# Performance work log

Hardware: AMD Instinct MI355X
Metric: run time of the kernel (lower is better)

The kernel has to match this reference:

```python
import jax, jax.numpy as jnp
import numpy as np

B, LQ, LK = 4, 2048, 2048
DQ, DK, DO = 1024, 1024, 1024


def setup_inputs() -> dict:
    key = jax.random.key(0)
    ks = jax.random.split(key, 9)
    s = 0.02
    return {
        "query_input": jax.random.normal(ks[0], (B, LQ, DQ), jnp.float32),
        "key_input": jax.random.normal(ks[1], (B, LK, DK), jnp.float32),
        "value_input": jax.random.normal(ks[2], (B, LK, DK), jnp.float32),
        "Wq": jax.random.normal(ks[3], (DQ, DO), jnp.float32) * s,
        "bq": jax.random.normal(ks[4], (DO,), jnp.float32) * s,
        "Wk": jax.random.normal(ks[5], (DK, DO), jnp.float32) * s,
        "bk": jax.random.normal(ks[6], (DO,), jnp.float32) * s,
        "Wv": jax.random.normal(ks[7], (DK, DO), jnp.float32) * s,
        "bv": jax.random.normal(ks[8], (DO,), jnp.float32) * s,
    }


def reference(query_input, key_input, value_input, Wq, bq, Wk, bk, Wv, bv):
    scale = jnp.asarray(DO, query_input.dtype) ** 0.5
    q = query_input @ Wq + bq              # [B, Lq, D]
    k = key_input @ Wk + bk                # [B, Lk, D]
    v = value_input @ Wv + bv              # [B, Lk, D]
    attn = jnp.einsum("bqd,bkd->bqk", q, k) / scale
    attn = jax.nn.softmax(attn, axis=-1)
    return jnp.einsum("bqk,bkd->bqd", attn, v)
```

## Files before the change

kernel.cpp:

```cpp
#include <hip/hip_runtime.h>

typedef _Float16 f16x8 __attribute__((ext_vector_type(8)));
typedef _Float16 f16x4 __attribute__((ext_vector_type(4)));
typedef float f32x4 __attribute__((ext_vector_type(4)));
typedef int   v4i   __attribute__((ext_vector_type(4)));

__device__ __forceinline__ void lds_load16(const _Float16* g, _Float16* l) {
    __builtin_amdgcn_global_load_lds(
        (const __attribute__((address_space(1))) void*)g,
        (__attribute__((address_space(3))) void*)l,
        16, 0, 0);
}

__device__ __forceinline__ f16x8 ldsr(unsigned a) {
    v4i r;
    asm volatile("ds_read_b128 %0, %1" : "=v"(r) : "v"(a));
    return __builtin_bit_cast(f16x8, r);
}

template <int MODE>
__global__ __launch_bounds__(512, 2)
void gemm_core(const _Float16* A0, const _Float16* B0, void* C0, const float* b0,
               const _Float16* A1, const _Float16* B1, void* C1, const float* b1,
               const _Float16* A2, const _Float16* B2, void* C2, const float* b2,
               float* rowsum)
{
    constexpr int BM  = (MODE == 5) ? 128 : 256;
    constexpr int K   = (MODE == 5) ? 2048 : 1024;
    constexpr int LDA = (MODE == 5) ? 2048 : 1024;
    constexpr int LDB = (MODE == 5) ? 8192 : 1024;
    constexpr int NT  = K / 64;
    constexpr int MI  = BM / 32;
    constexpr int MH  = MI / 2;
    constexpr int LA  = BM / 64;
    constexpr int LT  = LA + 4;

    __shared__ __align__(16) _Float16 As[2][BM * 64];
    __shared__ __align__(16) _Float16 Bs[2][256 * 64];

    const int z_ = blockIdx.z;
    const int bx = blockIdx.x, by = blockIdx.y;
    const int t    = threadIdx.x;
    const int w    = t >> 6;
    const int lane = t & 63;
    const int ln   = lane & 15;
    const int kq   = lane >> 4;
    const int wm   = (w >> 2) * (BM / 2);
    const int wn   = (w & 3) * 64;

    const _Float16* A;
    const _Float16* B;
    size_t cbase = 0;
    int m0, n0, z = z_;

    if (MODE == 0) {
        A = z == 0 ? A0 : z == 1 ? A1 : A2;
        B = z == 0 ? B0 : z == 1 ? B1 : B2;
        if (z == 2) { m0 = (by & 3) * 256;             n0 = (bx * 4 + (by >> 2)) * 256; }
        else        { m0 = (bx * 4 + (by >> 2)) * 256; n0 = (by & 3) * 256; }
    } else if (MODE == 3) {
        A = A0 + (size_t)z * 2048 * 1024;
        B = B0 + (size_t)z * 2048 * 1024;
        cbase = (size_t)z * 2048 * 2048;
        rowsum += z * 2048;
        m0 = ((bx & 3) * 2 + (by >> 2)) * 256;
        n0 = ((bx >> 2) * 4 + (by & 3)) * 256;
    } else {
        z = (blockIdx.z << 1) | (bx >> 2);
        A = A0 + (size_t)z * 2048 * 2048;
        B = B0 + (size_t)z * 2048;
        cbase = (size_t)z * 2048 * 1024;
        rowsum += z * 2048;
        m0 = by * 128;
        n0 = (bx & 3) * 256;
    }

    const int r6 = t >> 3;
    const int cw = ((t & 7) ^ (r6 & 7)) * 8;
    const _Float16* gA = A + (size_t)(m0 + r6) * LDA + cw;
    const _Float16* gB = B + (size_t)(n0 + r6) * LDB + cw;

    auto stA = [&](int b, int kt, int s) {
        lds_load16(gA + (size_t)(s * 64) * LDA + kt * 64, As[b] + s * 4096 + w * 512);
    };
    auto stB = [&](int b, int kt, int s) {
        lds_load16(gB + (size_t)(s * 64) * LDB + kt * 64, Bs[b] + s * 4096 + w * 512);
    };

    const int xr  = ln & 7;
    const int sk0 = ((0 + kq) ^ xr) * 8;
    const int sk1 = ((4 + kq) ^ xr) * 8;
    const int ra  = (wm + ln) * 64;
    const int rb  = (wn + ln) * 64;

    const unsigned uA0 = (unsigned)(uintptr_t)(__attribute__((address_space(3))) _Float16*)&As[0][0];
    const unsigned uA1 = (unsigned)(uintptr_t)(__attribute__((address_space(3))) _Float16*)&As[1][0];
    const unsigned uB0 = (unsigned)(uintptr_t)(__attribute__((address_space(3))) _Float16*)&Bs[0][0];
    const unsigned uB1 = (unsigned)(uintptr_t)(__attribute__((address_space(3))) _Float16*)&Bs[1][0];
    const unsigned aA[2][2] = { { uA0 + 2u * (ra + sk0), uA0 + 2u * (ra + sk1) },
                                { uA1 + 2u * (ra + sk0), uA1 + 2u * (ra + sk1) } };
    const unsigned aB[2][2] = { { uB0 + 2u * (rb + sk0), uB0 + 2u * (rb + sk1) },
                                { uB1 + 2u * (rb + sk0), uB1 + 2u * (rb + sk1) } };

    f16x8 af[MH][2], bf[4][2];
    f32x4 acc[MI][4] = {};

    {
#pragma unroll
        for (int s = 0; s < LA; ++s) stA(0, 0, s);
#pragma unroll
        for (int s = 0; s < 4; ++s)  stB(0, 0, s);
#pragma unroll
        for (int s = 0; s < LA; ++s) stA(1, 1, s);
#pragma unroll
        for (int s = 0; s < 4; ++s)  stB(1, 1, s);
    }
    if constexpr (MODE == 5) asm volatile("s_waitcnt vmcnt(6)" ::: "memory");
    else                     asm volatile("s_waitcnt vmcnt(8)" ::: "memory");
    __builtin_amdgcn_s_barrier();
    __builtin_amdgcn_sched_barrier(0);

#pragma unroll 2
    for (int kc = 0; kc < NT; ++kc) {
        const int  b  = kc & 1;
        const bool pf = (kc + 2 < NT);

#pragma unroll
        for (int i = 0; i < MH; ++i) {
            af[i][0] = ldsr(aA[b][0] + i * 2048);
            af[i][1] = ldsr(aA[b][1] + i * 2048);
        }
#pragma unroll
        for (int j = 0; j < 2; ++j) {
            bf[j][0] = ldsr(aB[b][0] + j * 2048);
            bf[j][1] = ldsr(aB[b][1] + j * 2048);
        }
        __builtin_amdgcn_s_barrier();
        asm volatile("s_waitcnt lgkmcnt(0)" ::: "memory");
        __builtin_amdgcn_sched_barrier(0);
        __builtin_amdgcn_s_setprio(1);
#pragma unroll
        for (int kh = 0; kh < 2; ++kh)
#pragma unroll
            for (int i = 0; i < MH; ++i)
#pragma unroll
                for (int j = 0; j < 2; ++j)
                    acc[i][j] = __builtin_amdgcn_mfma_f32_16x16x32_f16(af[i][kh], bf[j][kh], acc[i][j], 0, 0, 0);
        __builtin_amdgcn_s_setprio(0);
        __builtin_amdgcn_s_barrier();
        __builtin_amdgcn_sched_barrier(0);

#pragma unroll
        for (int j = 2; j < 4; ++j) {
            bf[j][0] = ldsr(aB[b][0] + j * 2048);
            bf[j][1] = ldsr(aB[b][1] + j * 2048);
        }
        if constexpr (LA == 4) {
            if (pf) { stA(b, kc + 2, 0); stA(b, kc + 2, 2); }
        }
        __builtin_amdgcn_s_barrier();
        asm volatile("s_waitcnt lgkmcnt(0)" ::: "memory");
        __builtin_amdgcn_sched_barrier(0);
        __builtin_amdgcn_s_setprio(1);
#pragma unroll
        for (int kh = 0; kh < 2; ++kh)
#pragma unroll
            for (int i = 0; i < MH; ++i)
#pragma unroll
                for (int j = 2; j < 4; ++j)
                    acc[i][j] = __builtin_amdgcn_mfma_f32_16x16x32_f16(af[i][kh], bf[j][kh], acc[i][j], 0, 0, 0);
        __builtin_amdgcn_s_setprio(0);
        __builtin_amdgcn_s_barrier();
        __builtin_amdgcn_sched_barrier(0);

#pragma unroll
        for (int i = 0; i < MH; ++i) {
            af[i][0] = ldsr(aA[b][0] + (i + MH) * 2048);
            af[i][1] = ldsr(aA[b][1] + (i + MH) * 2048);
        }
        if (pf) { stB(b, kc + 2, 0); stB(b, kc + 2, 1); stB(b, kc + 2, 2); }
        __builtin_amdgcn_s_barrier();
        asm volatile("s_waitcnt lgkmcnt(0)" ::: "memory");
        __builtin_amdgcn_sched_barrier(0);
        __builtin_amdgcn_s_setprio(1);
#pragma unroll
        for (int kh = 0; kh < 2; ++kh)
#pragma unroll
            for (int i = 0; i < MH; ++i)
#pragma unroll
                for (int j = 0; j < 2; ++j)
                    acc[i + MH][j] = __builtin_amdgcn_mfma_f32_16x16x32_f16(af[i][kh], bf[j][kh], acc[i + MH][j], 0, 0, 0);
        __builtin_amdgcn_s_setprio(0);
        __builtin_amdgcn_s_barrier();
        __builtin_amdgcn_sched_barrier(0);

        if (pf) {
            stB(b, kc + 2, 3);
            if constexpr (LA == 4) { stA(b, kc + 2, 1); stA(b, kc + 2, 3); }
            else                   { stA(b, kc + 2, 0); stA(b, kc + 2, 1); }
            if constexpr (MODE == 5) asm volatile("s_waitcnt vmcnt(6)" ::: "memory");
            else                     asm volatile("s_waitcnt vmcnt(8)" ::: "memory");
        } else if (kc + 1 < NT) {
            asm volatile("s_waitcnt vmcnt(0)" ::: "memory");
        }
        __builtin_amdgcn_s_barrier();
        __builtin_amdgcn_sched_barrier(0);
        __builtin_amdgcn_s_setprio(1);
#pragma unroll
        for (int kh = 0; kh < 2; ++kh)
#pragma unroll
            for (int i = 0; i < MH; ++i)
#pragma unroll
                for (int j = 2; j < 4; ++j)
                    acc[i + MH][j] = __builtin_amdgcn_mfma_f32_16x16x32_f16(af[i][kh], bf[j][kh], acc[i + MH][j], 0, 0, 0);
        __builtin_amdgcn_s_setprio(0);
        __builtin_amdgcn_s_barrier();
        __builtin_amdgcn_sched_barrier(0);
    }

    if (MODE == 0) {
        _Float16* Cp = (_Float16*)(z == 0 ? C0 : z == 1 ? C1 : C2);
        const float* bp = z == 0 ? b0 : z == 1 ? b1 : b2;
        const int ldc = (z == 2) ? 8192 : 1024;
#pragma unroll
        for (int i = 0; i < MI; ++i) {
            const int rbase = m0 + wm + i * 16 + kq * 4;
#pragma unroll
            for (int j = 0; j < 4; ++j) {
                const int gcol = n0 + wn + j * 16 + ln;
#pragma unroll
                for (int r = 0; r < 4; ++r) {
                    float vv = acc[i][j][r] + (z == 2 ? bp[rbase + r] : bp[gcol]);
                    Cp[(size_t)(rbase + r) * ldc + gcol] = (_Float16)vv;
                }
            }
        }
    } else if (MODE == 3) {
        _Float16* Ch = (_Float16*)C0;
#pragma unroll
        for (int i = 0; i < MI; ++i) {
            const int rbase = m0 + wm + i * 16 + kq * 4;
            float rs[4] = {0.f, 0.f, 0.f, 0.f};
#pragma unroll
            for (int j = 0; j < 4; ++j) {
                const int gcol = n0 + wn + j * 16 + ln;
#pragma unroll
                for (int r = 0; r < 4; ++r) {
                    float e = __expf(acc[i][j][r] * 0.03125f);
                    Ch[cbase + (size_t)(rbase + r) * 2048 + gcol] = (_Float16)e;
                    rs[r] += e;
                }
            }
#pragma unroll
            for (int r = 0; r < 4; ++r) {
                float s = rs[r];
                s += __shfl_xor(s, 1);
                s += __shfl_xor(s, 2);
                s += __shfl_xor(s, 4);
                s += __shfl_xor(s, 8);
                if (ln == 0) atomicAdd(&rowsum[rbase + r], s);
            }
        }
    } else {
        float* Cf = (float*)C0;
#pragma unroll
        for (int i = 0; i < MI; ++i) {
            const int rbase = m0 + wm + i * 16 + kq * 4;
            float inv[4];
#pragma unroll
            for (int r = 0; r < 4; ++r) inv[r] = 1.f / rowsum[rbase + r];
#pragma unroll
            for (int j = 0; j < 4; ++j) {
                const int gcol = n0 + wn + j * 16 + ln;
#pragma unroll
                for (int r = 0; r < 4; ++r)
                    Cf[cbase + (size_t)(rbase + r) * 1024 + gcol] = acc[i][j][r] * inv[r];
            }
        }
    }
}

__global__ __launch_bounds__(256)
void prep(const float4* __restrict__ x0, _Float16* __restrict__ y0,
          const float4* __restrict__ x1, _Float16* __restrict__ y1,
          const float4* __restrict__ x2, _Float16* __restrict__ y2,
          const float* __restrict__ W0, _Float16* __restrict__ T0,
          const float* __restrict__ W1, _Float16* __restrict__ T1,
          const float* __restrict__ W2, _Float16* __restrict__ T2,
          float* __restrict__ rowsum)
{
    if (blockIdx.y < 3) {
        const size_t i = (size_t)blockIdx.x * 256 + threadIdx.x;
        const float4* x = blockIdx.y == 0 ? x0 : blockIdx.y == 1 ? x1 : x2;
        _Float16*    yy = blockIdx.y == 0 ? y0 : blockIdx.y == 1 ? y1 : y2;
        float4 f = x[i];
        f16x4 o = { (_Float16)f.x, (_Float16)f.y, (_Float16)f.z, (_Float16)f.w };
        *(f16x4*)(yy + i * 4) = o;
        if (blockIdx.y == 0 && blockIdx.x < 32)
            rowsum[blockIdx.x * 256 + threadIdx.x] = 0.f;
        return;
    }
    if (blockIdx.x >= 3072) return;
    const int zz = blockIdx.x >> 10;
    const int tb = blockIdx.x & 1023;
    const float* W = zz == 0 ? W0 : zz == 1 ? W1 : W2;
    _Float16*   WT = zz == 0 ? T0 : zz == 1 ? T1 : T2;
    __shared__ float tile[32][33];
    const int bxs = (tb & 31) * 32;
    const int bys = (tb >> 5) * 32;
    const int tx = threadIdx.x & 31;
    const int ty = threadIdx.x >> 5;
#pragma unroll
    for (int i = ty; i < 32; i += 8)
        tile[i][tx] = W[(size_t)(bys + i) * 1024 + bxs + tx];
    __syncthreads();
#pragma unroll
    for (int i = ty; i < 32; i += 8)
        WT[(size_t)(bxs + i) * 1024 + bys + tx] = (_Float16)tile[tx][i];
}

extern "C" void kernel_launch(void* const* d_in, const int* in_sizes, int n_in,
                              void* d_out, int out_size, void* d_ws, size_t ws_size,
                              hipStream_t stream)
{
    const float* Xq = (const float*)d_in[0];
    const float* Xk = (const float*)d_in[1];
    const float* Xv = (const float*)d_in[2];
    const float* Wq = (const float*)d_in[3];
    const float* bq = (const float*)d_in[4];
    const float* Wk = (const float*)d_in[5];
    const float* bk = (const float*)d_in[6];
    const float* Wv = (const float*)d_in[7];
    const float* bv = (const float*)d_in[8];
    float* out = (float*)d_out;

    const size_t XN = (size_t)8192 * 1024;
    const size_t WN = (size_t)1024 * 1024;

    _Float16* ws  = (_Float16*)d_ws;
    _Float16* Xqh = ws;
    _Float16* Xkh = Xqh + XN;
    _Float16* Xvh = Xkh + XN;
    _Float16* WqT = Xvh + XN;
    _Float16* WkT = WqT + WN;
    _Float16* WvT = WkT + WN;
    _Float16* qh  = WvT + WN;
    _Float16* kh  = qh + XN;
    _Float16* vT  = kh + XN;
    _Float16* S   = vT + XN;
    float* rowsum = (float*)(S + (size_t)4 * 2048 * 2048);

    {
        dim3 g(8192, 4);
        prep<<<g, 256, 0, stream>>>((const float4*)Xq, Xqh,
                                    (const float4*)Xk, Xkh,
                                    (const float4*)Xv, Xvh,
                                    Wq, WqT, Wk, WkT, Wv, WvT, rowsum);
    }

    {
        dim3 g(8, 16, 3);
        gemm_core<0><<<g, 512, 0, stream>>>(
            Xqh, WqT, qh, bq,
            Xkh, WkT, kh, bk,
            WvT, Xvh, vT, bv,
            nullptr);
    }

    {
        dim3 g(8, 8, 4);
        gemm_core<3><<<g, 512, 0, stream>>>(
            qh, kh, S, nullptr,
            nullptr, nullptr, nullptr, nullptr,
            nullptr, nullptr, nullptr, nullptr,
            rowsum);
    }

    {
        dim3 g(8, 16, 2);
        gemm_core<5><<<g, 512, 0, stream>>>(
            S, vT, out, nullptr,
            nullptr, nullptr, nullptr, nullptr,
            nullptr, nullptr, nullptr, nullptr,
            rowsum);
    }
}
```

Baseline: 305.3 us.

## Add dedicated 128x128 triple-buffered projection GEMM kernel with smaller K tiles

The QKV projection GEMM moves out of the shared 256x256, 512-thread template into its own kernel. The new kernel uses 128x128 tiles, 256 threads, K-step 32 and a three-stage LDS ring buffer with global_load_lds prefetch two tiles ahead. This launches 1536 blocks instead of 384, to improve occupancy and CU load balance on the projection stage. The cost is lower data reuse per tile and more barriers per K step. The attention GEMMs are only cleaned up to drop the unused MODE 0 path.

```diff
diff --git a/kernel.cpp b/kernel.cpp
--- a/kernel.cpp
+++ b/kernel.cpp
@@ -17,13 +17,126 @@
     asm volatile("ds_read_b128 %0, %1" : "=v"(r) : "v"(a));
     return __builtin_bit_cast(f16x8, r);
 }
+template <int OFF>
+__device__ __forceinline__ f16x8 ldsrO(unsigned a) {
+    v4i r;
+    if constexpr (OFF == 0)
+        asm volatile("ds_read_b128 %0, %1" : "=v"(r) : "v"(a));
+    else
+        asm volatile("ds_read_b128 %0, %1 offset:%2" : "=v"(r) : "v"(a), "i"(OFF));
+    return __builtin_bit_cast(f16x8, r);
+}
+
+__global__ __launch_bounds__(256, 3)
+void gemm_proj(const _Float16* A0, const _Float16* B0, void* C0, const float* b0,
+               const _Float16* A1, const _Float16* B1, void* C1, const float* b1,
+               const _Float16* A2, const _Float16* B2, void* C2, const float* b2)
+{
+    constexpr int K = 1024, LDA = 1024, LDB = 1024, NT = K / 32;
+
+    __shared__ __align__(16) _Float16 As[3][128 * 32];
+    __shared__ __align__(16) _Float16 Bs[3][128 * 32];
+
+    const int z  = blockIdx.z;
+    const int bx = blockIdx.x, by = blockIdx.y;
+    const int t    = threadIdx.x;
+    const int w    = t >> 6;
+    const int lane = t & 63;
+    const int ln   = lane & 15;
+    const int kq   = lane >> 4;
+    const int wm   = (w & 1) * 64;
+    const int wn   = (w >> 1) * 64;
+
+    const _Float16* A = z == 0 ? A0 : z == 1 ? A1 : A2;
+    const _Float16* B = z == 0 ? B0 : z == 1 ? B1 : B2;
+    int m0, n0;
+    if (z == 2) { m0 = (by & 7) * 128; n0 = (bx * 8 + (by >> 3)) * 128; }
+    else        { m0 = (bx * 8 + (by >> 3)) * 128; n0 = (by & 7) * 128; }
+
+    const int r4 = t >> 2;
+    const int sc = ((t & 3) ^ ((t >> 3) & 3)) * 8;
+    const _Float16* gA = A + (size_t)(m0 + r4) * LDA + sc;
+    const _Float16* gB = B + (size_t)(n0 + r4) * LDB + sc;
+    _Float16* const lA = &As[0][0] + w * 512;
+    _Float16* const lB = &Bs[0][0] + w * 512;
+
+    auto stage = [&](unsigned bufE, int kt) {
+        lds_load16(gA + kt * 32,                     lA + bufE);
+        lds_load16(gA + (size_t)64 * LDA + kt * 32,  lA + bufE + 2048);
+        lds_load16(gB + kt * 32,                     lB + bufE);
+        lds_load16(gB + (size_t)64 * LDB + kt * 32,  lB + bufE + 2048);
+    };
+
+    const int sk = (kq ^ ((ln >> 1) & 3)) * 16;
+    const unsigned uA0 = (unsigned)(uintptr_t)(__attribute__((address_space(3))) _Float16*)&As[0][0];
+    const unsigned uB0 = (unsigned)(uintptr_t)(__attribute__((address_space(3))) _Float16*)&Bs[0][0];
+    const unsigned vAbase = uA0 + (wm + ln) * 64 + sk;
+    const unsigned vBbase = uB0 + (wn + ln) * 64 + sk;
+
+    f32x4 acc[4][4] = {};
+
+    stage(0, 0);
+    stage(4096, 1);
+    asm volatile("s_waitcnt vmcnt(4)" ::: "memory");
+    __builtin_amdgcn_s_barrier();
+    __builtin_amdgcn_sched_barrier(0);
+
+    unsigned offR = 0;
+    unsigned offW = 8192;
+
+    for (int kc = 0; kc < NT; ++kc) {
+        const unsigned aA = vAbase + offR;
+        const unsigned aB = vBbase + offR;
+        f16x8 af[4], bf[4];
+        af[0] = ldsrO<0>(aA);    af[1] = ldsrO<1024>(aA);
+        af[2] = ldsrO<2048>(aA); af[3] = ldsrO<3072>(aA);
+        bf[0] = ldsrO<0>(aB);    bf[1] = ldsrO<1024>(aB);
+        bf[2] = ldsrO<2048>(aB); bf[3] = ldsrO<3072>(aB);
+
+        const bool pf = (kc + 2 < NT);
+        if (pf) stage(offW, kc + 2);
+
+        asm volatile("s_waitcnt lgkmcnt(0)" ::: "memory");
+        __builtin_amdgcn_sched_barrier(0);
+        __builtin_amdgcn_s_setprio(1);
+#pragma unroll
+        for (int i = 0; i < 4; ++i)
+#pragma unroll
+            for (int j = 0; j < 4; ++j)
+                acc[i][j] = __builtin_amdgcn_mfma_f32_16x16x32_f16(af[i], bf[j], acc[i][j], 0, 0, 0);
+        __builtin_amdgcn_s_setprio(0);
+        __builtin_amdgcn_sched_barrier(0);
+
+        if (pf) asm volatile("s_waitcnt vmcnt(4)" ::: "memory");
+        else    asm volatile("s_waitcnt vmcnt(0)" ::: "memory");
+        __builtin_amdgcn_s_barrier();
+        __builtin_amdgcn_sched_barrier(0);
+
+        offR = (offR == 16384u) ? 0u : offR + 8192u;
+        offW = (offW == 8192u)  ? 0u : offW + 4096u;
+    }
+
+    _Float16* Cp = (_Float16*)(z == 0 ? C0 : z == 1 ? C1 : C2);
+    const float* bp = z == 0 ? b0 : z == 1 ? b1 : b2;
+    const int ldc = (z == 2) ? 8192 : 1024;
+#pragma unroll
+    for (int i = 0; i < 4; ++i) {
+        const int rbase = m0 + wm + i * 16 + kq * 4;
+#pragma unroll
+        for (int j = 0; j < 4; ++j) {
+            const int gcol = n0 + wn + j * 16 + ln;
+#pragma unroll
+            for (int r = 0; r < 4; ++r) {
+                float vv = acc[i][j][r] + (z == 2 ? bp[rbase + r] : bp[gcol]);
+                Cp[(size_t)(rbase + r) * ldc + gcol] = (_Float16)vv;
+            }
+        }
+    }
+}
 
 template <int MODE>
 __global__ __launch_bounds__(512, 2)
-void gemm_core(const _Float16* A0, const _Float16* B0, void* C0, const float* b0,
-               const _Float16* A1, const _Float16* B1, void* C1, const float* b1,
-               const _Float16* A2, const _Float16* B2, void* C2, const float* b2,
-               float* rowsum)
+void gemm_attn(const _Float16* A0, const _Float16* B0, void* C0, float* rowsum)
 {
     constexpr int BM  = (MODE == 5) ? 128 : 256;
     constexpr int K   = (MODE == 5) ? 2048 : 1024;
@@ -33,12 +146,10 @@
     constexpr int MI  = BM / 32;
     constexpr int MH  = MI / 2;
     constexpr int LA  = BM / 64;
-    constexpr int LT  = LA + 4;
 
     __shared__ __align__(16) _Float16 As[2][BM * 64];
     __shared__ __align__(16) _Float16 Bs[2][256 * 64];
 
-    const int z_ = blockIdx.z;
     const int bx = blockIdx.x, by = blockIdx.y;
     const int t    = threadIdx.x;
     const int w    = t >> 6;
@@ -51,14 +162,10 @@
     const _Float16* A;
     const _Float16* B;
     size_t cbase = 0;
-    int m0, n0, z = z_;
-
-    if (MODE == 0) {
-        A = z == 0 ? A0 : z == 1 ? A1 : A2;
-        B = z == 0 ? B0 : z == 1 ? B1 : B2;
-        if (z == 2) { m0 = (by & 3) * 256;             n0 = (bx * 4 + (by >> 2)) * 256; }
-        else        { m0 = (bx * 4 + (by >> 2)) * 256; n0 = (by & 3) * 256; }
-    } else if (MODE == 3) {
+    int m0, n0, z;
+
+    if (MODE == 3) {
+        z = blockIdx.z;
         A = A0 + (size_t)z * 2048 * 1024;
         B = B0 + (size_t)z * 2048 * 1024;
         cbase = (size_t)z * 2048 * 2048;
@@ -218,24 +325,7 @@
         __builtin_amdgcn_sched_barrier(0);
     }
 
-    if (MODE == 0) {
-        _Float16* Cp = (_Float16*)(z == 0 ? C0 : z == 1 ? C1 : C2);
-        const float* bp = z == 0 ? b0 : z == 1 ? b1 : b2;
-        const int ldc = (z == 2) ? 8192 : 1024;
-#pragma unroll
-        for (int i = 0; i < MI; ++i) {
-            const int rbase = m0 + wm + i * 16 + kq * 4;
-#pragma unroll
-            for (int j = 0; j < 4; ++j) {
-                const int gcol = n0 + wn + j * 16 + ln;
-#pragma unroll
-                for (int r = 0; r < 4; ++r) {
-                    float vv = acc[i][j][r] + (z == 2 ? bp[rbase + r] : bp[gcol]);
-                    Cp[(size_t)(rbase + r) * ldc + gcol] = (_Float16)vv;
-                }
-            }
-        }
-    } else if (MODE == 3) {
+    if (MODE == 3) {
         _Float16* Ch = (_Float16*)C0;
 #pragma unroll
         for (int i = 0; i < MI; ++i) {
@@ -359,29 +449,20 @@
     }
 
     {
-        dim3 g(8, 16, 3);
-        gemm_core<0><<<g, 512, 0, stream>>>(
+        dim3 g(8, 64, 3);
+        gemm_proj<<<g, 256, 0, stream>>>(
             Xqh, WqT, qh, bq,
             Xkh, WkT, kh, bk,
-            WvT, Xvh, vT, bv,
-            nullptr);
+            WvT, Xvh, vT, bv);
     }
 
     {
         dim3 g(8, 8, 4);
-        gemm_core<3><<<g, 512, 0, stream>>>(
-            qh, kh, S, nullptr,
-            nullptr, nullptr, nullptr, nullptr,
-            nullptr, nullptr, nullptr, nullptr,
-            rowsum);
+        gemm_attn<3><<<g, 512, 0, stream>>>(qh, kh, S, rowsum);
     }
 
     {
         dim3 g(8, 16, 2);
-        gemm_core<5><<<g, 512, 0, stream>>>(
-            S, vT, out, nullptr,
-            nullptr, nullptr, nullptr, nullptr,
-            nullptr, nullptr, nullptr, nullptr,
-            rowsum);
-    }
-}
+        gemm_attn<5><<<g, 512, 0, stream>>>(S, vT, out, rowsum);
+    }
+}
```

Result: faster. 298.9 us (-2.1%).
